# Performance work log

Hardware: AMD Instinct MI355X
Metric: run time of the kernel (lower is better)

The kernel has to match this reference:

```python
import jax, jax.numpy as jnp
import numpy as np

EMBED_DIM = 384
HIDDEN_DIM = 512
CODEBOOK_SIZE = 256
NUM_QUANTIZERS = 4
COMMIT_WEIGHT = 0.25
BATCH = 65536


def setup_inputs() -> dict:
    key = jax.random.key(0)
    ks = jax.random.split(key, 10)
    s_in = 1.0 / np.sqrt(EMBED_DIM)
    s_h = 1.0 / np.sqrt(HIDDEN_DIM)
    return {
        "x": jax.random.normal(ks[0], (BATCH, EMBED_DIM), jnp.float32),
        "enc_w1": jax.random.uniform(ks[1], (EMBED_DIM, HIDDEN_DIM), jnp.float32, -s_in, s_in),
        "enc_b1": jnp.zeros((HIDDEN_DIM,), jnp.float32),
        "enc_w2": jax.random.uniform(ks[2], (HIDDEN_DIM, HIDDEN_DIM), jnp.float32, -s_h, s_h),
        "enc_b2": jnp.zeros((HIDDEN_DIM,), jnp.float32),
        "codebooks": jax.random.normal(ks[3], (NUM_QUANTIZERS, CODEBOOK_SIZE, HIDDEN_DIM), jnp.float32),
        "dec_w1": jax.random.uniform(ks[4], (HIDDEN_DIM, HIDDEN_DIM), jnp.float32, -s_h, s_h),
        "dec_b1": jnp.zeros((HIDDEN_DIM,), jnp.float32),
        "dec_w2": jax.random.uniform(ks[5], (HIDDEN_DIM, EMBED_DIM), jnp.float32, -s_h, s_h),
        "dec_b2": jnp.zeros((EMBED_DIM,), jnp.float32),
    }


def _residual_vq(z, codebooks):
    """Sequential residual VQ with straight-through estimator and commitment loss.
    z: [B, D]; codebooks: [Q, K, D]. Returns quantized [B, D], indices [B, Q], commit_loss scalar."""
    residual = z
    quantized_out = jnp.zeros_like(z)
    commit_loss = jnp.asarray(0.0, z.dtype)
    idx_list = []
    for q in range(NUM_QUANTIZERS):
        cb = codebooks[q]  # [K, D]
        # nearest code: argmin ||r - c||^2 == argmax (2 r.c - ||c||^2)
        scores = 2.0 * (residual @ cb.T) - jnp.sum(cb * cb, axis=-1)  # [B, K]
        idx = jnp.argmax(scores, axis=-1)  # [B]
        quant = cb[idx]  # [B, D] gather
        commit_loss = commit_loss + COMMIT_WEIGHT * jnp.mean(
            (residual - jax.lax.stop_gradient(quant)) ** 2)
        # straight-through: value = quant, gradient flows to residual
        quant_st = residual + jax.lax.stop_gradient(quant - residual)
        quantized_out = quantized_out + quant_st
        residual = residual - jax.lax.stop_gradient(quant)
        idx_list.append(idx)
    indices = jnp.stack(idx_list, axis=-1)  # [B, Q]
    return quantized_out, indices, commit_loss


def reference(x, enc_w1, enc_b1, enc_w2, enc_b2, codebooks,
              dec_w1, dec_b1, dec_w2, dec_b2):
    # encoder MLP
    z = jax.nn.relu(x @ enc_w1 + enc_b1) @ enc_w2 + enc_b2  # [B, H]
    quantized, indices, commit_loss = _residual_vq(z, codebooks)
    # decoder MLP
    recon = jax.nn.relu(quantized @ dec_w1 + dec_b1) @ dec_w2 + dec_b2  # [B, E]
    recon_loss = jnp.mean((recon - x) ** 2)
    return recon, indices, recon_loss, commit_loss
```

## Files before the change

### kernel.cpp

```cpp
#include <hip/hip_runtime.h>
#include <cfloat>
#include <cstddef>


#define BATCH   65536
#define EDIM    384
#define HDIM    512
#define NCODE   256
#define NQ      4

#define OUT_IDX_OFF 25165824
#define OUT_RL_OFF  25427968
#define WS_BUFA     0
#define WS_BUFB     33554432
#define WS_CBSPL    67108864
#define WS_CNORM    67633152
#define WS_COMMITP  67634176
#define WS_RECONP   67636224
#define WS_W1S      67637760
#define WS_W2S      67834368
#define WS_W3S      68096512
#define WS_W4S      68358656

typedef _Float16 half8 __attribute__((ext_vector_type(8)));
typedef float    f32x16 __attribute__((ext_vector_type(16)));
typedef short    short8 __attribute__((ext_vector_type(8)));

__global__ __launch_bounds__(256)
void split_w(const float* __restrict__ W, unsigned short* __restrict__ out,
             int N, int K)
{
    int u = blockIdx.x * 256 + threadIdx.x;
    int col  = u % N;
    int rem  = u / N;
    int khalf = rem & 1;
    int kt    = rem >> 1;
    int kbase = kt * 16 + khalf * 8;
    half8 h, l;
#pragma unroll
    for (int j = 0; j < 8; ++j) {
        float v = W[(size_t)(kbase + j) * N + col];
        _Float16 hv = (_Float16)v;
        h[j] = hv;
        l[j] = (_Float16)(v - (float)hv);
    }
    size_t eh = ((size_t)(kt * 4 + khalf)) * N + col;
    size_t el = ((size_t)(kt * 4 + 2 + khalf)) * N + col;
    *reinterpret_cast<half8*>(out + eh * 8) = h;
    *reinterpret_cast<half8*>(out + el * 8) = l;
}

template <int BN, bool RELU, bool LOSS>
__global__ __launch_bounds__(256, 2)
void gemm_mfma(const float* __restrict__ A, const unsigned short* __restrict__ Wsp,
               const float* __restrict__ bias, float* __restrict__ C,
               const float* __restrict__ X, float* __restrict__ lossP,
               int N, int K)
{
    constexpr int WN = BN / 128;
    constexpr int WM = 4 / WN;
    constexpr int MR = 128 / WM;
    constexpr int FM = MR / 32;
    constexpr int LOG_BN = (BN == 256) ? 8 : 7;

    __shared__ __align__(16) _Float16 Ab[2][2][2][128][8];
    __shared__ __align__(16) _Float16 Bb[2][2][2][BN][8];
    __shared__ float red[256];

    const int tid  = threadIdx.x;
    const int wid  = tid >> 6;
    const int lane = tid & 63;
    const int l31  = lane & 31;
    const int lh   = lane >> 5;
    const int wm   = wid / WN;
    const int wn   = wid % WN;
    const int row0 = blockIdx.y * 128;
    const int n0   = blockIdx.x * BN;
    const int nkt  = K / 16;

    f32x16 acc[FM][4];
#pragma unroll
    for (int m = 0; m < FM; ++m)
#pragma unroll
        for (int n = 0; n < 4; ++n) acc[m][n] = (f32x16)(0.0f);

    const int arow = tid >> 1;
    const int akh  = tid & 1;

    auto stageB = [&](int db, int kt) {
        const short8* src = reinterpret_cast<const short8*>(Wsp) + (size_t)kt * 4 * N;
        short8* dst = reinterpret_cast<short8*>(&Bb[db][0][0][0][0]);
#pragma unroll
        for (int i = 0; i < BN / 64; ++i) {
            int e    = i * 256 + tid;
            int hlkh = e >> LOG_BN;
            int col  = e & (BN - 1);
            dst[e] = src[(size_t)hlkh * N + n0 + col];
        }
    };
    auto loadA = [&](int kt, float4& a0, float4& a1) {
        const float* p = A + (size_t)(row0 + arow) * K + kt * 16 + akh * 8;
        a0 = *reinterpret_cast<const float4*>(p);
        a1 = *reinterpret_cast<const float4*>(p + 4);
    };
    auto writeA = [&](int db, float4 a0, float4 a1) {
        float vs[8] = {a0.x, a0.y, a0.z, a0.w, a1.x, a1.y, a1.z, a1.w};
        half8 h, l;
#pragma unroll
        for (int j = 0; j < 8; ++j) {
            _Float16 hv = (_Float16)vs[j];
            h[j] = hv;
            l[j] = (_Float16)(vs[j] - (float)hv);
        }
        *reinterpret_cast<half8*>(&Ab[db][0][akh][arow][0]) = h;
        *reinterpret_cast<half8*>(&Ab[db][1][akh][arow][0]) = l;
    };

    {
        float4 ra0, ra1;
        loadA(0, ra0, ra1);
        stageB(0, 0);
        writeA(0, ra0, ra1);
        loadA(1, ra0, ra1);
        stageB(1, 1);
        writeA(1, ra0, ra1);
    }

    float4 pa0, pa1;
    for (int kt = 0; kt < nkt; ++kt) {
        const int db = kt & 1;
        __syncthreads();
        if (kt + 2 < nkt) loadA(kt + 2, pa0, pa1);

        half8 Ah[FM], Al[FM];
#pragma unroll
        for (int fm = 0; fm < FM; ++fm) {
            const int rb = wm * MR + fm * 32 + l31;
            Ah[fm] = *reinterpret_cast<const half8*>(&Ab[db][0][lh][rb][0]);
            Al[fm] = *reinterpret_cast<const half8*>(&Ab[db][1][lh][rb][0]);
        }
#pragma unroll
        for (int nt = 0; nt < 4; ++nt) {
            const int col = wn * 128 + nt * 32 + l31;
            half8 Bh = *reinterpret_cast<const half8*>(&Bb[db][0][lh][col][0]);
            half8 Bl = *reinterpret_cast<const half8*>(&Bb[db][1][lh][col][0]);
#pragma unroll
            for (int fm = 0; fm < FM; ++fm) {
                acc[fm][nt] = __builtin_amdgcn_mfma_f32_32x32x16_f16(Ah[fm], Bh, acc[fm][nt], 0, 0, 0);
                acc[fm][nt] = __builtin_amdgcn_mfma_f32_32x32x16_f16(Ah[fm], Bl, acc[fm][nt], 0, 0, 0);
                acc[fm][nt] = __builtin_amdgcn_mfma_f32_32x32x16_f16(Al[fm], Bh, acc[fm][nt], 0, 0, 0);
            }
        }
        __syncthreads();
        if (kt + 2 < nkt) { stageB(db, kt + 2); writeA(db, pa0, pa1); }
    }

    float lacc = 0.f;
#pragma unroll
    for (int fm = 0; fm < FM; ++fm) {
#pragma unroll
        for (int nt = 0; nt < 4; ++nt) {
            const int col = n0 + wn * 128 + nt * 32 + l31;
            const float b = bias[col];
#pragma unroll
            for (int rg = 0; rg < 16; ++rg) {
                const int row = row0 + wm * MR + fm * 32 + (rg & 3) + 8 * (rg >> 2) + 4 * lh;
                float v = acc[fm][nt][rg] + b;
                if (RELU) v = v > 0.f ? v : 0.f;
                C[(size_t)row * N + col] = v;
                if constexpr (LOSS) {
                    float d = v - X[(size_t)row * N + col];
                    lacc = fmaf(d, d, lacc);
                }
            }
        }
    }

    if constexpr (LOSS) {
        red[tid] = lacc;
        __syncthreads();
        for (int s = 128; s > 0; s >>= 1) {
            if (tid < s) red[tid] += red[tid + s];
            __syncthreads();
        }
        if (tid == 0) lossP[blockIdx.y * gridDim.x + blockIdx.x] = red[0];
    }
}

__global__ __launch_bounds__(64)
void cnorm_kernel(const float* __restrict__ cb, float* __restrict__ cnorm)
{
    const int code = blockIdx.x;
    const int lane = threadIdx.x;
    const float* r = cb + (size_t)code * HDIM;
    float s = 0.f;
    for (int k = lane; k < HDIM; k += 64) s = fmaf(r[k], r[k], s);
#pragma unroll
    for (int off = 32; off > 0; off >>= 1) s += __shfl_down(s, off);
    if (lane == 0) cnorm[code] = s;
}

__global__ __launch_bounds__(256)
void split_cb(const float* __restrict__ cb, unsigned short* __restrict__ out)
{
    int u = blockIdx.x * 256 + threadIdx.x;
    int q    = u >> 14;
    int rem  = u & 16383;
    int code = rem >> 6;
    int kt   = (rem >> 1) & 31;
    int khalf = rem & 1;
    int k = kt * 16 + khalf * 8;
    const float* p = cb + ((size_t)(q * NCODE + code)) * HDIM + k;
    float4 v0 = *reinterpret_cast<const float4*>(p);
    float4 v1 = *reinterpret_cast<const float4*>(p + 4);
    float vs[8] = {v0.x, v0.y, v0.z, v0.w, v1.x, v1.y, v1.z, v1.w};
    half8 h, l;
#pragma unroll
    for (int j = 0; j < 8; ++j) {
        _Float16 hv = (_Float16)vs[j];
        h[j] = hv;
        l[j] = (_Float16)(vs[j] - (float)hv);
    }
    size_t o = (size_t)(q * 32 + kt) * 8192 + (size_t)khalf * 2048 + (size_t)code * 8;
    *reinterpret_cast<half8*>(out + o)        = h;
    *reinterpret_cast<half8*>(out + o + 4096) = l;
}

template <bool LAST>
__global__ __launch_bounds__(256, 2)
void vq_stage(int q,
              const float* Rin, float* Rout, const float* zsrc,
              const unsigned short* __restrict__ cbs,
              const float* __restrict__ cb,
              const float* __restrict__ cnorm,
              float* __restrict__ idx_out,
              float* __restrict__ commitP)
{
    __shared__ __align__(16) _Float16 Ab[2][2][2][128][8];
    __shared__ __align__(16) _Float16 Bb[2][2][2][256][8];
    __shared__ float sval[2][128];
    __shared__ int   sidx[2][128];
    __shared__ int   idxbuf[128];
    __shared__ float red[256];

    const int tid  = threadIdx.x;
    const int wid  = tid >> 6;
    const int lane = tid & 63;
    const int l31  = lane & 31;
    const int lh   = lane >> 5;
    const int wm   = wid >> 1;
    const int wn   = wid & 1;
    const int row0 = blockIdx.x * 128;

    f32x16 acc[2][4];
#pragma unroll
    for (int m = 0; m < 2; ++m)
#pragma unroll
        for (int n = 0; n < 4; ++n) acc[m][n] = (f32x16)(0.0f);

    const int arow = tid >> 1;
    const int akh  = tid & 1;

    auto stageB = [&](int db, int kt) {
        const short8* src = reinterpret_cast<const short8*>(cbs + (size_t)(q * 32 + kt) * 8192);
        short8* dst = reinterpret_cast<short8*>(&Bb[db][0][0][0][0]);
#pragma unroll
        for (int i = 0; i < 4; ++i)
            dst[i * 256 + tid] = src[i * 256 + tid];
    };
    auto loadA = [&](int kt, float4& a0, float4& a1) {
        const float* p = Rin + (size_t)(row0 + arow) * HDIM + kt * 16 + akh * 8;
        a0 = *reinterpret_cast<const float4*>(p);
        a1 = *reinterpret_cast<const float4*>(p + 4);
    };
    auto writeA = [&](int db, float4 a0, float4 a1) {
        float vs[8] = {a0.x, a0.y, a0.z, a0.w, a1.x, a1.y, a1.z, a1.w};
        half8 h, l;
#pragma unroll
        for (int j = 0; j < 8; ++j) {
            _Float16 hv = (_Float16)vs[j];
            h[j] = hv;
            l[j] = (_Float16)(vs[j] - (float)hv);
        }
        *reinterpret_cast<half8*>(&Ab[db][0][akh][arow][0]) = h;
        *reinterpret_cast<half8*>(&Ab[db][1][akh][arow][0]) = l;
    };

    {
        float4 ra0, ra1;
        loadA(0, ra0, ra1);
        stageB(0, 0);
        writeA(0, ra0, ra1);
        loadA(1, ra0, ra1);
        stageB(1, 1);
        writeA(1, ra0, ra1);
    }

    float4 pa0, pa1;
    for (int kt = 0; kt < 32; ++kt) {
        const int db = kt & 1;
        __syncthreads();
        if (kt + 2 < 32) loadA(kt + 2, pa0, pa1);

        const int rb = wm * 64 + l31;
        half8 Ah0 = *reinterpret_cast<const half8*>(&Ab[db][0][lh][rb][0]);
        half8 Al0 = *reinterpret_cast<const half8*>(&Ab[db][1][lh][rb][0]);
        half8 Ah1 = *reinterpret_cast<const half8*>(&Ab[db][0][lh][rb + 32][0]);
        half8 Al1 = *reinterpret_cast<const half8*>(&Ab[db][1][lh][rb + 32][0]);
#pragma unroll
        for (int nt = 0; nt < 4; ++nt) {
            const int code = wn * 128 + nt * 32 + l31;
            half8 Bh = *reinterpret_cast<const half8*>(&Bb[db][0][lh][code][0]);
            half8 Bl = *reinterpret_cast<const half8*>(&Bb[db][1][lh][code][0]);
            acc[0][nt] = __builtin_amdgcn_mfma_f32_32x32x16_f16(Ah0, Bh, acc[0][nt], 0, 0, 0);
            acc[0][nt] = __builtin_amdgcn_mfma_f32_32x32x16_f16(Ah0, Bl, acc[0][nt], 0, 0, 0);
            acc[0][nt] = __builtin_amdgcn_mfma_f32_32x32x16_f16(Al0, Bh, acc[0][nt], 0, 0, 0);
            acc[1][nt] = __builtin_amdgcn_mfma_f32_32x32x16_f16(Ah1, Bh, acc[1][nt], 0, 0, 0);
            acc[1][nt] = __builtin_amdgcn_mfma_f32_32x32x16_f16(Ah1, Bl, acc[1][nt], 0, 0, 0);
            acc[1][nt] = __builtin_amdgcn_mfma_f32_32x32x16_f16(Al1, Bh, acc[1][nt], 0, 0, 0);
        }
        __syncthreads();
        if (kt + 2 < 32) { stageB(db, kt + 2); writeA(db, pa0, pa1); }
    }

    const float* cn = cnorm + q * NCODE;
#pragma unroll
    for (int Mt = 0; Mt < 2; ++Mt) {
#pragma unroll
        for (int rg = 0; rg < 16; ++rg) {
            float bv = -FLT_MAX;
            int   bi = 0;
#pragma unroll
            for (int nt = 0; nt < 4; ++nt) {
                const int code = wn * 128 + nt * 32 + l31;
                float s = 2.f * acc[Mt][nt][rg] - cn[code];
                if (s > bv || (s == bv && code < bi)) { bv = s; bi = code; }
            }
#pragma unroll
            for (int m = 1; m < 32; m <<= 1) {
                float ov = __shfl_xor(bv, m, 64);
                int   oi = __shfl_xor(bi, m, 64);
                if (ov > bv || (ov == bv && oi < bi)) { bv = ov; bi = oi; }
            }
            if (l31 == 0) {
                int row = wm * 64 + Mt * 32 + (rg & 3) + 8 * (rg >> 2) + 4 * lh;
                sval[wn][row] = bv;
                sidx[wn][row] = bi;
            }
        }
    }
    __syncthreads();
    if (tid < 128) {
        float v0 = sval[0][tid], v1 = sval[1][tid];
        int   i0 = sidx[0][tid], i1 = sidx[1][tid];
        int b = (v1 > v0 || (v1 == v0 && i1 < i0)) ? i1 : i0;
        idxbuf[tid] = b;
        idx_out[(size_t)(row0 + tid) * NQ + q] = (float)b;
    }
    __syncthreads();

    float ca = 0.f;
    const int rgrp = tid >> 3;
    const int lpos = tid & 7;
#pragma unroll
    for (int rr = 0; rr < 4; ++rr) {
        const int row = rr * 32 + rgrp;
        const float* rin  = Rin + (size_t)(row0 + row) * HDIM;
        const float* crow = cb + ((size_t)q * NCODE + idxbuf[row]) * HDIM;
        float* rout = Rout + (size_t)(row0 + row) * HDIM;
        const float* zr = LAST ? (zsrc + (size_t)(row0 + row) * HDIM) : nullptr;
#pragma unroll
        for (int j = 0; j < 16; ++j) {
            const int f4 = lpos + j * 8;
            float4 rv = *reinterpret_cast<const float4*>(rin + f4 * 4);
            float4 cv = *reinterpret_cast<const float4*>(crow + f4 * 4);
            float4 d;
            d.x = rv.x - cv.x; d.y = rv.y - cv.y;
            d.z = rv.z - cv.z; d.w = rv.w - cv.w;
            ca = fmaf(d.x, d.x, ca); ca = fmaf(d.y, d.y, ca);
            ca = fmaf(d.z, d.z, ca); ca = fmaf(d.w, d.w, ca);
            if constexpr (LAST) {
                float4 zv = *reinterpret_cast<const float4*>(zr + f4 * 4);
                float4 qv;
                qv.x = zv.x - d.x; qv.y = zv.y - d.y;
                qv.z = zv.z - d.z; qv.w = zv.w - d.w;
                *reinterpret_cast<float4*>(rout + f4 * 4) = qv;
            } else {
                *reinterpret_cast<float4*>(rout + f4 * 4) = d;
            }
        }
    }

    red[tid] = ca;
    __syncthreads();
    for (int s = 128; s > 0; s >>= 1) {
        if (tid < s) red[tid] += red[tid + s];
        __syncthreads();
    }
    if (tid == 0) commitP[q * 512 + blockIdx.x] = red[0];
}

__global__ __launch_bounds__(256)
void loss_reduce(const float* __restrict__ cP, int nc,
                 const float* __restrict__ rP, int nr,
                 float* __restrict__ out2)
{
    __shared__ float red[256];
    const int tid = threadIdx.x;

    float s = 0.f;
    for (int i = tid; i < nc; i += 256) s += cP[i];
    red[tid] = s;
    __syncthreads();
    for (int st = 128; st > 0; st >>= 1) {
        if (tid < st) red[tid] += red[tid + st];
        __syncthreads();
    }
    float ctot = red[0];
    __syncthreads();

    s = 0.f;
    for (int i = tid; i < nr; i += 256) s += rP[i];
    red[tid] = s;
    __syncthreads();
    for (int st = 128; st > 0; st >>= 1) {
        if (tid < st) red[tid] += red[tid + st];
        __syncthreads();
    }
    if (tid == 0) {
        out2[0] = red[0] / ((float)BATCH * (float)EDIM);
        out2[1] = 0.25f * ctot / ((float)BATCH * (float)HDIM);
    }
}

extern "C" void kernel_launch(void* const* d_in, const int* in_sizes, int n_in,
                              void* d_out, int out_size, void* d_ws, size_t ws_size,
                              hipStream_t stream)
{
    const float* x   = (const float*)d_in[0];
    const float* ew1 = (const float*)d_in[1];
    const float* eb1 = (const float*)d_in[2];
    const float* ew2 = (const float*)d_in[3];
    const float* eb2 = (const float*)d_in[4];
    const float* cb  = (const float*)d_in[5];
    const float* dw1 = (const float*)d_in[6];
    const float* db1 = (const float*)d_in[7];
    const float* dw2 = (const float*)d_in[8];
    const float* db2 = (const float*)d_in[9];

    float* out  = (float*)d_out;
    float* ws   = (float*)d_ws;
    float* bufA = ws + WS_BUFA;
    float* bufB = ws + WS_BUFB;
    unsigned short* cbs = (unsigned short*)(ws + WS_CBSPL);
    float* cn   = ws + WS_CNORM;
    float* cP   = ws + WS_COMMITP;
    float* rP   = ws + WS_RECONP;
    unsigned short* w1s = (unsigned short*)(ws + WS_W1S);
    unsigned short* w2s = (unsigned short*)(ws + WS_W2S);
    unsigned short* w3s = (unsigned short*)(ws + WS_W3S);
    unsigned short* w4s = (unsigned short*)(ws + WS_W4S);

    cnorm_kernel<<<NQ * NCODE, 64, 0, stream>>>(cb, cn);
    split_cb<<<256, 256, 0, stream>>>(cb, cbs);
    split_w<<<(EDIM / 16) * 2 * HDIM / 256, 256, 0, stream>>>(ew1, w1s, HDIM, EDIM);
    split_w<<<(HDIM / 16) * 2 * HDIM / 256, 256, 0, stream>>>(ew2, w2s, HDIM, HDIM);
    split_w<<<(HDIM / 16) * 2 * HDIM / 256, 256, 0, stream>>>(dw1, w3s, HDIM, HDIM);
    split_w<<<(HDIM / 16) * 2 * EDIM / 256, 256, 0, stream>>>(dw2, w4s, EDIM, HDIM);

    gemm_mfma<256, true, false><<<dim3(HDIM / 256, BATCH / 128), 256, 0, stream>>>(
        x, w1s, eb1, bufA, nullptr, nullptr, HDIM, EDIM);
    gemm_mfma<256, false, false><<<dim3(HDIM / 256, BATCH / 128), 256, 0, stream>>>(
        bufA, w2s, eb2, bufB, nullptr, nullptr, HDIM, HDIM);

    float* idxo = out + OUT_IDX_OFF;
    vq_stage<false><<<512, 256, 0, stream>>>(0, bufB, bufA, nullptr, cbs, cb, cn, idxo, cP);
    vq_stage<false><<<512, 256, 0, stream>>>(1, bufA, bufA, nullptr, cbs, cb, cn, idxo, cP);
    vq_stage<false><<<512, 256, 0, stream>>>(2, bufA, bufA, nullptr, cbs, cb, cn, idxo, cP);
    vq_stage<true ><<<512, 256, 0, stream>>>(3, bufA, bufB, bufB,    cbs, cb, cn, idxo, cP);

    gemm_mfma<256, true, false><<<dim3(HDIM / 256, BATCH / 128), 256, 0, stream>>>(
        bufB, w3s, db1, bufA, nullptr, nullptr, HDIM, HDIM);
    gemm_mfma<128, false, true><<<dim3(EDIM / 128, BATCH / 128), 256, 0, stream>>>(
        bufA, w4s, db2, out, x, rP, EDIM, HDIM);

    loss_reduce<<<1, 256, 0, stream>>>(cP, NQ * 512, rP,
                                       (BATCH / 128) * (EDIM / 128),
                                       out + OUT_RL_OFF);
}
```

Measured before the change: 972.9 us.

## Load GEMM and VQ operands directly from global memory into registers, dropping LDS staging

Removes the double-buffered shared-memory staging of A and B tiles in both the GEMM and VQ kernels. Each wave now loads its own A rows and pre-split fp16 B fragments from global memory straight into registers, with no block barriers in the k-loop. This eliminates LDS traffic and __syncthreads, but A rows are redundantly loaded and hi/lo-split by every wave sharing them. It also loses explicit prefetching and relies on L1/L2 caching and unrolling to hide global latency.

Result: slower. 1.046 ms (+7.5%).

```diff
diff --git a/kernel.cpp b/kernel.cpp
--- a/kernel.cpp
+++ b/kernel.cpp
@@ -24,7 +24,18 @@
 
 typedef _Float16 half8 __attribute__((ext_vector_type(8)));
 typedef float    f32x16 __attribute__((ext_vector_type(16)));
-typedef short    short8 __attribute__((ext_vector_type(8)));
+
+__device__ __forceinline__ void cvt_hl(const float4& a0, const float4& a1,
+                                       half8& h, half8& l)
+{
+    float vs[8] = {a0.x, a0.y, a0.z, a0.w, a1.x, a1.y, a1.z, a1.w};
+#pragma unroll
+    for (int j = 0; j < 8; ++j) {
+        _Float16 hv = (_Float16)vs[j];
+        h[j] = hv;
+        l[j] = (_Float16)(vs[j] - (float)hv);
+    }
+}
 
 __global__ __launch_bounds__(256)
 void split_w(const float* __restrict__ W, unsigned short* __restrict__ out,
@@ -52,20 +63,15 @@
 
 template <int BN, bool RELU, bool LOSS>
 __global__ __launch_bounds__(256, 2)
-void gemm_mfma(const float* __restrict__ A, const unsigned short* __restrict__ Wsp,
-               const float* __restrict__ bias, float* __restrict__ C,
-               const float* __restrict__ X, float* __restrict__ lossP,
-               int N, int K)
+void gemm_reg(const float* __restrict__ A, const unsigned short* __restrict__ Wsp,
+              const float* __restrict__ bias, float* __restrict__ C,
+              const float* __restrict__ X, float* __restrict__ lossP,
+              int N, int K)
 {
     constexpr int WN = BN / 128;
     constexpr int WM = 4 / WN;
     constexpr int MR = 128 / WM;
     constexpr int FM = MR / 32;
-    constexpr int LOG_BN = (BN == 256) ? 8 : 7;
-
-    __shared__ __align__(16) _Float16 Ab[2][2][2][128][8];
-    __shared__ __align__(16) _Float16 Bb[2][2][2][BN][8];
-    __shared__ float red[256];
 
     const int tid  = threadIdx.x;
     const int wid  = tid >> 6;
@@ -84,66 +90,29 @@
 #pragma unroll
         for (int n = 0; n < 4; ++n) acc[m][n] = (f32x16)(0.0f);
 
-    const int arow = tid >> 1;
-    const int akh  = tid & 1;
-
-    auto stageB = [&](int db, int kt) {
-        const short8* src = reinterpret_cast<const short8*>(Wsp) + (size_t)kt * 4 * N;
-        short8* dst = reinterpret_cast<short8*>(&Bb[db][0][0][0][0]);
-#pragma unroll
-        for (int i = 0; i < BN / 64; ++i) {
-            int e    = i * 256 + tid;
-            int hlkh = e >> LOG_BN;
-            int col  = e & (BN - 1);
-            dst[e] = src[(size_t)hlkh * N + n0 + col];
-        }
-    };
-    auto loadA = [&](int kt, float4& a0, float4& a1) {
-        const float* p = A + (size_t)(row0 + arow) * K + kt * 16 + akh * 8;
-        a0 = *reinterpret_cast<const float4*>(p);
-        a1 = *reinterpret_cast<const float4*>(p + 4);
-    };
-    auto writeA = [&](int db, float4 a0, float4 a1) {
-        float vs[8] = {a0.x, a0.y, a0.z, a0.w, a1.x, a1.y, a1.z, a1.w};
-        half8 h, l;
-#pragma unroll
-        for (int j = 0; j < 8; ++j) {
-            _Float16 hv = (_Float16)vs[j];
-            h[j] = hv;
-            l[j] = (_Float16)(vs[j] - (float)hv);
-        }
-        *reinterpret_cast<half8*>(&Ab[db][0][akh][arow][0]) = h;
-        *reinterpret_cast<half8*>(&Ab[db][1][akh][arow][0]) = l;
-    };
-
-    {
-        float4 ra0, ra1;
-        loadA(0, ra0, ra1);
-        stageB(0, 0);
-        writeA(0, ra0, ra1);
-        loadA(1, ra0, ra1);
-        stageB(1, 1);
-        writeA(1, ra0, ra1);
-    }
-
-    float4 pa0, pa1;
+    const float* ap[FM];
+#pragma unroll
+    for (int fm = 0; fm < FM; ++fm)
+        ap[fm] = A + (size_t)(row0 + wm * MR + fm * 32 + l31) * K + lh * 8;
+
+    const half8* b8 = reinterpret_cast<const half8*>(Wsp);
+    const int colb = n0 + wn * 128 + l31;
+
+#pragma unroll 2
     for (int kt = 0; kt < nkt; ++kt) {
-        const int db = kt & 1;
-        __syncthreads();
-        if (kt + 2 < nkt) loadA(kt + 2, pa0, pa1);
-
         half8 Ah[FM], Al[FM];
 #pragma unroll
         for (int fm = 0; fm < FM; ++fm) {
-            const int rb = wm * MR + fm * 32 + l31;
-            Ah[fm] = *reinterpret_cast<const half8*>(&Ab[db][0][lh][rb][0]);
-            Al[fm] = *reinterpret_cast<const half8*>(&Ab[db][1][lh][rb][0]);
-        }
+            float4 a0 = *reinterpret_cast<const float4*>(ap[fm] + kt * 16);
+            float4 a1 = *reinterpret_cast<const float4*>(ap[fm] + kt * 16 + 4);
+            cvt_hl(a0, a1, Ah[fm], Al[fm]);
+        }
+        const size_t eh = (size_t)(kt * 4 + lh) * N + colb;
+        const size_t el = (size_t)(kt * 4 + 2 + lh) * N + colb;
 #pragma unroll
         for (int nt = 0; nt < 4; ++nt) {
-            const int col = wn * 128 + nt * 32 + l31;
-            half8 Bh = *reinterpret_cast<const half8*>(&Bb[db][0][lh][col][0]);
-            half8 Bl = *reinterpret_cast<const half8*>(&Bb[db][1][lh][col][0]);
+            half8 Bh = b8[eh + nt * 32];
+            half8 Bl = b8[el + nt * 32];
 #pragma unroll
             for (int fm = 0; fm < FM; ++fm) {
                 acc[fm][nt] = __builtin_amdgcn_mfma_f32_32x32x16_f16(Ah[fm], Bh, acc[fm][nt], 0, 0, 0);
@@ -151,8 +120,6 @@
                 acc[fm][nt] = __builtin_amdgcn_mfma_f32_32x32x16_f16(Al[fm], Bh, acc[fm][nt], 0, 0, 0);
             }
         }
-        __syncthreads();
-        if (kt + 2 < nkt) { stageB(db, kt + 2); writeA(db, pa0, pa1); }
     }
 
     float lacc = 0.f;
@@ -177,6 +144,7 @@
     }
 
     if constexpr (LOSS) {
+        __shared__ float red[256];
         red[tid] = lacc;
         __syncthreads();
         for (int s = 128; s > 0; s >>= 1) {
@@ -213,14 +181,8 @@
     const float* p = cb + ((size_t)(q * NCODE + code)) * HDIM + k;
     float4 v0 = *reinterpret_cast<const float4*>(p);
     float4 v1 = *reinterpret_cast<const float4*>(p + 4);
-    float vs[8] = {v0.x, v0.y, v0.z, v0.w, v1.x, v1.y, v1.z, v1.w};
     half8 h, l;
-#pragma unroll
-    for (int j = 0; j < 8; ++j) {
-        _Float16 hv = (_Float16)vs[j];
-        h[j] = hv;
-        l[j] = (_Float16)(vs[j] - (float)hv);
-    }
+    cvt_hl(v0, v1, h, l);
     size_t o = (size_t)(q * 32 + kt) * 8192 + (size_t)khalf * 2048 + (size_t)code * 8;
     *reinterpret_cast<half8*>(out + o)        = h;
     *reinterpret_cast<half8*>(out + o + 4096) = l;
@@ -229,15 +191,14 @@
 template <bool LAST>
 __global__ __launch_bounds__(256, 2)
 void vq_stage(int q,
-              const float* Rin, float* Rout, const float* zsrc,
+              const float* __restrict__ Rin, float* __restrict__ Rout,
+              const float* __restrict__ zsrc,
               const unsigned short* __restrict__ cbs,
               const float* __restrict__ cb,
               const float* __restrict__ cnorm,
               float* __restrict__ idx_out,
               float* __restrict__ commitP)
 {
-    __shared__ __align__(16) _Float16 Ab[2][2][2][128][8];
-    __shared__ __align__(16) _Float16 Bb[2][2][2][256][8];
     __shared__ float sval[2][128];
     __shared__ int   sidx[2][128];
     __shared__ int   idxbuf[128];
@@ -258,69 +219,36 @@
 #pragma unroll
         for (int n = 0; n < 4; ++n) acc[m][n] = (f32x16)(0.0f);
 
-    const int arow = tid >> 1;
-    const int akh  = tid & 1;
-
-    auto stageB = [&](int db, int kt) {
-        const short8* src = reinterpret_cast<const short8*>(cbs + (size_t)(q * 32 + kt) * 8192);
-        short8* dst = reinterpret_cast<short8*>(&Bb[db][0][0][0][0]);
-#pragma unroll
-        for (int i = 0; i < 4; ++i)
-            dst[i * 256 + tid] = src[i * 256 + tid];
-    };
-    auto loadA = [&](int kt, float4& a0, float4& a1) {
-        const float* p = Rin + (size_t)(row0 + arow) * HDIM + kt * 16 + akh * 8;
-        a0 = *reinterpret_cast<const float4*>(p);
-        a1 = *reinterpret_cast<const float4*>(p + 4);
-    };
-    auto writeA = [&](int db, float4 a0, float4 a1) {
-        float vs[8] = {a0.x, a0.y, a0.z, a0.w, a1.x, a1.y, a1.z, a1.w};
-        half8 h, l;
-#pragma unroll
-        for (int j = 0; j < 8; ++j) {
-            _Float16 hv = (_Float16)vs[j];
-            h[j] = hv;
-            l[j] = (_Float16)(vs[j] - (float)hv);
-        }
-        *reinterpret_cast<half8*>(&Ab[db][0][akh][arow][0]) = h;
-        *reinterpret_cast<half8*>(&Ab[db][1][akh][arow][0]) = l;
-    };
-
-    {
-        float4 ra0, ra1;
-        loadA(0, ra0, ra1);
-        stageB(0, 0);
-        writeA(0, ra0, ra1);
-        loadA(1, ra0, ra1);
-        stageB(1, 1);
-        writeA(1, ra0, ra1);
-    }
-
-    float4 pa0, pa1;
+    const float* ap[2];
+#pragma unroll
+    for (int fm = 0; fm < 2; ++fm)
+        ap[fm] = Rin + (size_t)(row0 + wm * 64 + fm * 32 + l31) * HDIM + lh * 8;
+
+    const half8* c8 = reinterpret_cast<const half8*>(cbs);
+    const size_t qbase = (size_t)q * 32 * 1024;
+    const int code_b = wn * 128 + l31;
+
+#pragma unroll 4
     for (int kt = 0; kt < 32; ++kt) {
-        const int db = kt & 1;
-        __syncthreads();
-        if (kt + 2 < 32) loadA(kt + 2, pa0, pa1);
-
-        const int rb = wm * 64 + l31;
-        half8 Ah0 = *reinterpret_cast<const half8*>(&Ab[db][0][lh][rb][0]);
-        half8 Al0 = *reinterpret_cast<const half8*>(&Ab[db][1][lh][rb][0]);
-        half8 Ah1 = *reinterpret_cast<const half8*>(&Ab[db][0][lh][rb + 32][0]);
-        half8 Al1 = *reinterpret_cast<const half8*>(&Ab[db][1][lh][rb + 32][0]);
+        half8 Ah[2], Al[2];
+#pragma unroll
+        for (int fm = 0; fm < 2; ++fm) {
+            float4 a0 = *reinterpret_cast<const float4*>(ap[fm] + kt * 16);
+            float4 a1 = *reinterpret_cast<const float4*>(ap[fm] + kt * 16 + 4);
+            cvt_hl(a0, a1, Ah[fm], Al[fm]);
+        }
+        const size_t eh = qbase + (size_t)kt * 1024 + (size_t)lh * 256 + code_b;
 #pragma unroll
         for (int nt = 0; nt < 4; ++nt) {
-            const int code = wn * 128 + nt * 32 + l31;
-            half8 Bh = *reinterpret_cast<const half8*>(&Bb[db][0][lh][code][0]);
-            half8 Bl = *reinterpret_cast<const half8*>(&Bb[db][1][lh][code][0]);
-            acc[0][nt] = __builtin_amdgcn_mfma_f32_32x32x16_f16(Ah0, Bh, acc[0][nt], 0, 0, 0);
-            acc[0][nt] = __builtin_amdgcn_mfma_f32_32x32x16_f16(Ah0, Bl, acc[0][nt], 0, 0, 0);
-            acc[0][nt] = __builtin_amdgcn_mfma_f32_32x32x16_f16(Al0, Bh, acc[0][nt], 0, 0, 0);
-            acc[1][nt] = __builtin_amdgcn_mfma_f32_32x32x16_f16(Ah1, Bh, acc[1][nt], 0, 0, 0);
-            acc[1][nt] = __builtin_amdgcn_mfma_f32_32x32x16_f16(Ah1, Bl, acc[1][nt], 0, 0, 0);
-            acc[1][nt] = __builtin_amdgcn_mfma_f32_32x32x16_f16(Al1, Bh, acc[1][nt], 0, 0, 0);
-        }
-        __syncthreads();
-        if (kt + 2 < 32) { stageB(db, kt + 2); writeA(db, pa0, pa1); }
+            half8 Bh = c8[eh + nt * 32];
+            half8 Bl = c8[eh + 512 + nt * 32];
+#pragma unroll
+            for (int fm = 0; fm < 2; ++fm) {
+                acc[fm][nt] = __builtin_amdgcn_mfma_f32_32x32x16_f16(Ah[fm], Bh, acc[fm][nt], 0, 0, 0);
+                acc[fm][nt] = __builtin_amdgcn_mfma_f32_32x32x16_f16(Ah[fm], Bl, acc[fm][nt], 0, 0, 0);
+                acc[fm][nt] = __builtin_amdgcn_mfma_f32_32x32x16_f16(Al[fm], Bh, acc[fm][nt], 0, 0, 0);
+            }
+        }
     }
 
     const float* cn = cnorm + q * NCODE;
@@ -468,9 +396,9 @@
     split_w<<<(HDIM / 16) * 2 * HDIM / 256, 256, 0, stream>>>(dw1, w3s, HDIM, HDIM);
     split_w<<<(HDIM / 16) * 2 * EDIM / 256, 256, 0, stream>>>(dw2, w4s, EDIM, HDIM);
 
-    gemm_mfma<256, true, false><<<dim3(HDIM / 256, BATCH / 128), 256, 0, stream>>>(
+    gemm_reg<256, true, false><<<dim3(HDIM / 256, BATCH / 128), 256, 0, stream>>>(
         x, w1s, eb1, bufA, nullptr, nullptr, HDIM, EDIM);
-    gemm_mfma<256, false, false><<<dim3(HDIM / 256, BATCH / 128), 256, 0, stream>>>(
+    gemm_reg<256, false, false><<<dim3(HDIM / 256, BATCH / 128), 256, 0, stream>>>(
         bufA, w2s, eb2, bufB, nullptr, nullptr, HDIM, HDIM);
 
     float* idxo = out + OUT_IDX_OFF;
@@ -479,9 +407,9 @@
     vq_stage<false><<<512, 256, 0, stream>>>(2, bufA, bufA, nullptr, cbs, cb, cn, idxo, cP);
     vq_stage<true ><<<512, 256, 0, stream>>>(3, bufA, bufB, bufB,    cbs, cb, cn, idxo, cP);
 
-    gemm_mfma<256, true, false><<<dim3(HDIM / 256, BATCH / 128), 256, 0, stream>>>(
+    gemm_reg<256, true, false><<<dim3(HDIM / 256, BATCH / 128), 256, 0, stream>>>(
         bufB, w3s, db1, bufA, nullptr, nullptr, HDIM, HDIM);
-    gemm_mfma<128, false, true><<<dim3(EDIM / 128, BATCH / 128), 256, 0, stream>>>(
+    gemm_reg<128, false, true><<<dim3(EDIM / 128, BATCH / 128), 256, 0, stream>>>(
         bufA, w4s, db2, out, x, rP, EDIM, HDIM);
 
     loss_reduce<<<1, 256, 0, stream>>>(cP, NQ * 512, rP,
```
